# Optimization experiments

Hardware: AMD Instinct MI355X
Metric: run time of the kernel (lower is better)

## Reference

```python
import jax, jax.numpy as jnp
import numpy as np

KH, KW = 3, 3
SH, SW = 1, 1
IC, OC = 32, 32
M = 4
P = M * M
ITERS = 3
LAM = 1.0
EPS = 1e-8


def _patches(t, kh, kw, sh, sw):
    # t: [B, H, W, ...] -> [B, Ho, Wo, kh, kw, ...] (im2col, matches torch unfold+permute)
    H, W = t.shape[1], t.shape[2]
    Ho = (H - kh) // sh + 1
    Wo = (W - kw) // sw + 1
    i = (jnp.arange(Ho) * sh)[:, None] + jnp.arange(kh)[None, :]  # [Ho,kh]
    j = (jnp.arange(Wo) * sw)[:, None] + jnp.arange(kw)[None, :]  # [Wo,kw]
    tp = t[:, i]            # [B,Ho,kh,W,...]
    tp = tp[:, :, :, j]     # [B,Ho,kh,Wo,kw,...]
    return jnp.moveaxis(tp, 2, 3)  # [B,Ho,Wo,kh,kw,...]


def setup_inputs() -> dict:
    key = jax.random.key(0)
    k1, k2, k3, k4, k5 = jax.random.split(key, 5)
    x = jax.random.normal(k1, (4, 14, 14, IC, M, M), dtype=jnp.float32)
    a = jax.random.uniform(k2, (4, 14, 14, IC), dtype=jnp.float32)
    W = jax.random.uniform(k3, (KH, KW, IC, OC, M, M), dtype=jnp.float32)   # torch.rand init
    beta_u = jax.random.uniform(k4, (1, OC, 1), dtype=jnp.float32)
    beta_a = jax.random.uniform(k5, (1, OC), dtype=jnp.float32)
    return {"x": x, "a": a, "W": W, "beta_u": beta_u, "beta_a": beta_a}


def reference(x, a, W, beta_u, beta_a):
    # im2col patches
    xp = _patches(x, KH, KW, SH, SW)          # [B,Ho,Wo,kh,kw,IC,M,M]
    ap = _patches(a, KH, KW, SH, SW)          # [B,Ho,Wo,kh,kw,IC]
    # pose-transform votes: per (kh,kw,inCap,outCap) 4x4 matmul
    V = jnp.einsum('bhwklcxy,klcoyz->bhwklcoxz', xp, W)
    B, Ho, Wo = V.shape[:3]
    N = KH * KW * IC
    V = V.reshape(B, Ho, Wo, N, OC, P)        # votes
    a_in = ap.reshape(B, Ho, Wo, N)
    bu = beta_u.reshape(OC, 1)
    ba = beta_a.reshape(OC)

    # EM routing (Hinton et al. 2018, fixed inverse temperature)
    R = jnp.full((B, Ho, Wo, N, OC), 1.0 / OC, dtype=V.dtype)
    for it in range(ITERS):
        Ra = R * a_in[..., None]                                  # [B,Ho,Wo,N,OC]
        Rs = Ra.sum(axis=3) + EPS                                 # [B,Ho,Wo,OC]
        mu = jnp.einsum('bhwno,bhwnop->bhwop', Ra, V) / Rs[..., None]
        d = V - mu[:, :, :, None]                                 # [B,Ho,Wo,N,OC,P]
        sig2 = jnp.einsum('bhwno,bhwnop->bhwop', Ra, d * d) / Rs[..., None] + EPS
        cost = (bu + 0.5 * jnp.log(sig2)) * Rs[..., None]         # [B,Ho,Wo,OC,P]
        a_out = jax.nn.sigmoid(LAM * (ba - cost.sum(-1)))         # [B,Ho,Wo,OC]
        if it < ITERS - 1:
            logp = -0.5 * jnp.sum(d * d / sig2[:, :, :, None] + jnp.log(sig2)[:, :, :, None], axis=-1)
            R = jax.nn.softmax(jnp.log(a_out + EPS)[:, :, :, None] + logp, axis=-1)

    pose = mu.reshape(B, Ho, Wo, OC, M, M)
    return pose, a_out
```

## Files before the change

### kernel.cpp

```cpp
#include <hip/hip_runtime.h>


#define EPSV 1e-8f

template <int CTRL>
__device__ __forceinline__ float dppf(float v) {
  return __int_as_float(__builtin_amdgcn_update_dpp(
      0, __float_as_int(v), CTRL, 0xf, 0xf, true));
}
__device__ __forceinline__ float swz16(float v) {
  return __int_as_float(__builtin_amdgcn_ds_swizzle(__float_as_int(v), 0x401F));
}
__device__ __forceinline__ float red_max32(float v) {
  v = fmaxf(v, dppf<0xB1>(v));
  v = fmaxf(v, dppf<0x4E>(v));
  v = fmaxf(v, dppf<0x141>(v));
  v = fmaxf(v, dppf<0x140>(v));
  v = fmaxf(v, swz16(v));
  return v;
}
__device__ __forceinline__ float red_sum32(float v) {
  v += dppf<0xB1>(v);
  v += dppf<0x4E>(v);
  v += dppf<0x141>(v);
  v += dppf<0x140>(v);
  v += swz16(v);
  return v;
}

__device__ __forceinline__ void compute_votes(const float* __restrict__ Wt,
                                              const float* __restrict__ xr,
                                              int n, int o, float* __restrict__ V)
{
  float Wf[16];
  {
    const float* wp = Wt + (((n << 5) + o) << 4);
#pragma unroll
    for (int i = 0; i < 4; ++i) {
      const float4 q = *(const float4*)(wp + (i << 2));
      Wf[i*4+0]=q.x; Wf[i*4+1]=q.y; Wf[i*4+2]=q.z; Wf[i*4+3]=q.w;
    }
  }
  float xv[16];
#pragma unroll
  for (int i = 0; i < 4; ++i) {
    const float4 q = *(const float4*)(xr + (i << 2));
    xv[i*4+0]=q.x; xv[i*4+1]=q.y; xv[i*4+2]=q.z; xv[i*4+3]=q.w;
  }
#pragma unroll
  for (int xi = 0; xi < 4; ++xi)
#pragma unroll
    for (int z = 0; z < 4; ++z)
      V[xi*4+z] = fmaf(xv[xi*4+0], Wf[z],
                  fmaf(xv[xi*4+1], Wf[4+z],
                  fmaf(xv[xi*4+2], Wf[8+z],
                       xv[xi*4+3]* Wf[12+z])));
}

__global__ __launch_bounds__(512, 4) void caps_stats(
    const float* __restrict__ X, const float* __restrict__ A, const float* __restrict__ Wt,
    const float* __restrict__ Bu, const float* __restrict__ Ba,
    const float* __restrict__ prev, float* __restrict__ cur, int it)
{
  __shared__ float xp_s[144*16];
  __shared__ float a_s[144];
  __shared__ float part[8*544];
  __shared__ float prs[8*32];
  __shared__ float mu_t[512], isig_t[512], lsig_t[512];
  __shared__ float la_s[32], slog_s[32], rs_s[32];

  const int t    = threadIdx.x;
  const int o    = t & 31;
  const int ng   = t >> 5;
  const int wv   = t >> 6;
  const int lane = t & 63;

  const int bid  = blockIdx.x;
  const int pos  = bid >> 1;
  const int half = bid & 1;
  const int b  = pos / 144;
  const int r_ = pos - b*144;
  const int h  = r_ / 12;
  const int w  = r_ - (r_/12)*12;
  const int nbase = half * 144;

  for (int i = t; i < 576; i += 512) {
    const int r  = i >> 2, q4 = i & 3;
    const int n  = nbase + r;
    const int kl = n >> 5, c = n & 31;
    const int hy = h + kl/3, wx = w + (kl - (kl/3)*3);
    const float4 v = *(const float4*)(X + ((((b*14+hy)*14+wx) << 9) + (c << 4) + (q4 << 2)));
    *(float4*)(xp_s + (r << 4) + (q4 << 2)) = v;
  }
  if (t < 144) {
    const int n  = nbase + t;
    const int kl = n >> 5, c = n & 31;
    const int hy = h + kl/3, wx = w + (kl - (kl/3)*3);
    a_s[t] = A[((b*14+hy)*14+wx)*32 + c];
  }

  float mu_r[16], isig_r[16];
  float la_r = 0.f, slog_r = 0.f;

  if (it > 0) {
    {
      const int pi = t >> 5, oo = t & 31;
      const float* h0 = prev + (pos*2+0)*1056;
      const float* h1 = prev + (pos*2+1)*1056;
      const int idx = pi*32 + oo;
      const float s1   = h0[idx]       + h1[idx];
      const float s2   = h0[512+idx]   + h1[512+idx];
      const float rsum = h0[1024+oo]   + h1[1024+oo] + EPSV;
      const float mu = s1 / rsum;
      float var = s2 / rsum - mu*mu;
      var = fmaxf(var, 0.f);
      const float sg = var + EPSV;
      mu_t[idx]   = mu;
      isig_t[idx] = 1.0f / sg;
      lsig_t[idx] = __logf(sg);
      if (pi == 0) rs_s[oo] = rsum;
    }
    __syncthreads();
    if (t < 32) {
      float slog = 0.f;
#pragma unroll
      for (int p = 0; p < 16; ++p) slog += lsig_t[p*32 + t];
      const float cost = rs_s[t] * (16.0f*Bu[t] + 0.5f*slog);
      const float av = 1.0f / (1.0f + __expf(-(Ba[t] - cost)));
      la_s[t]   = __logf(av + EPSV);
      slog_s[t] = slog;
    }
    __syncthreads();
#pragma unroll
    for (int p = 0; p < 16; ++p) { mu_r[p] = mu_t[p*32 + o]; isig_r[p] = isig_t[p*32 + o]; }
    slog_r = slog_s[o];
    la_r   = la_s[o];
  } else {
#pragma unroll
    for (int p = 0; p < 16; ++p) { mu_r[p] = 0.f; isig_r[p] = 0.f; }
    __syncthreads();
  }

  float S1[16], S2[16];
#pragma unroll
  for (int p = 0; p < 16; ++p) { S1[p] = 0.f; S2[p] = 0.f; }
  float rs = 0.f;

#pragma unroll 1
  for (int j = 0; j < 9; ++j) {
    const int nl = ng + (j << 4);
    const int n  = nbase + nl;
    float V[16];
    compute_votes(Wt, xp_s + (nl << 4), n, o, V);

    float ra;
    if (it == 0) {
      ra = a_s[nl] * (1.0f/32.0f);
    } else {
      float q0 = 0.f, q1 = 0.f, q2 = 0.f, q3 = 0.f;
#pragma unroll
      for (int p = 0; p < 4; ++p) {
        float d;
        d = V[p]    - mu_r[p];    q0 = fmaf(d*d, isig_r[p],    q0);
        d = V[p+4]  - mu_r[p+4];  q1 = fmaf(d*d, isig_r[p+4],  q1);
        d = V[p+8]  - mu_r[p+8];  q2 = fmaf(d*d, isig_r[p+8],  q2);
        d = V[p+12] - mu_r[p+12]; q3 = fmaf(d*d, isig_r[p+12], q3);
      }
      const float q = slog_r + ((q0 + q1) + (q2 + q3));
      const float z = la_r - 0.5f*q;
      const float m  = red_max32(z);
      const float ev = __expf(z - m);
      const float s  = red_sum32(ev);
      ra = (ev / s) * a_s[nl];
    }
    rs += ra;
#pragma unroll
    for (int p = 0; p < 16; ++p) {
      const float rv = ra * V[p];
      S1[p] += rv;
      S2[p] = fmaf(rv, V[p], S2[p]);
    }
  }

#pragma unroll
  for (int p = 0; p < 16; ++p) {
    S1[p] += __shfl_xor(S1[p], 32);
    S2[p] += __shfl_xor(S2[p], 32);
  }
  rs += __shfl_xor(rs, 32);

  float* dst = cur + bid*1056;

  if (lane < 32) {
    float* p1 = part + wv*544 + o*17;
#pragma unroll
    for (int p = 0; p < 16; ++p) p1[p] = S1[p];
    prs[wv*32 + o] = rs;
  }
  __syncthreads();
  {
    const int pi = t >> 5, oo = t & 31;
    float s1 = 0.f;
#pragma unroll
    for (int g = 0; g < 8; ++g) s1 += part[g*544 + oo*17 + pi];
    dst[t] = s1;
    if (t < 32) {
      float r = 0.f;
#pragma unroll
      for (int g = 0; g < 8; ++g) r += prs[(g << 5) + t];
      dst[1024 + t] = r;
    }
  }
  __syncthreads();

  if (lane < 32) {
    float* p2 = part + wv*544 + o*17;
#pragma unroll
    for (int p = 0; p < 16; ++p) p2[p] = S2[p];
  }
  __syncthreads();
  {
    const int pi = t >> 5, oo = t & 31;
    float s2 = 0.f;
#pragma unroll
    for (int g = 0; g < 8; ++g) s2 += part[g*544 + oo*17 + pi];
    dst[512 + t] = s2;
  }
}

__global__ __launch_bounds__(512, 4) void caps_final(
    const float* __restrict__ prev, const float* __restrict__ Bu,
    const float* __restrict__ Ba, float* __restrict__ Out)
{
  __shared__ float mu_t[512], lsig_t[512], rs_s[32], aout_s[32];

  const int t   = threadIdx.x;
  const int pos = blockIdx.x;
  {
    const int pi = t >> 5, oo = t & 31;
    const float* h0 = prev + (pos*2+0)*1056;
    const float* h1 = prev + (pos*2+1)*1056;
    const int idx = pi*32 + oo;
    const float s1   = h0[idx]     + h1[idx];
    const float s2   = h0[512+idx] + h1[512+idx];
    const float rsum = h0[1024+oo] + h1[1024+oo] + EPSV;
    const float mu = s1 / rsum;
    float var = s2 / rsum - mu*mu;
    var = fmaxf(var, 0.f);
    mu_t[idx]   = mu;
    lsig_t[idx] = __logf(var + EPSV);
    if (pi == 0) rs_s[oo] = rsum;
  }
  __syncthreads();
  if (t < 32) {
    float slog = 0.f;
#pragma unroll
    for (int p = 0; p < 16; ++p) slog += lsig_t[p*32 + t];
    const float cost = rs_s[t] * (16.0f*Bu[t] + 0.5f*slog);
    aout_s[t] = 1.0f / (1.0f + __expf(-(Ba[t] - cost)));
  }
  __syncthreads();
  {
    const int oo = t >> 4, pi = t & 15;
    Out[pos*512 + t] = mu_t[pi*32 + oo];
  }
  if (t < 32) Out[294912 + pos*32 + t] = aout_s[t];
}

extern "C" void kernel_launch(void* const* d_in, const int* in_sizes, int n_in,
                              void* d_out, int out_size, void* d_ws, size_t ws_size,
                              hipStream_t stream) {
  (void)in_sizes; (void)n_in; (void)ws_size; (void)out_size;
  const float* X  = (const float*)d_in[0];
  const float* A  = (const float*)d_in[1];
  const float* Wt = (const float*)d_in[2];
  const float* Bu = (const float*)d_in[3];
  const float* Ba = (const float*)d_in[4];
  float* Out = (float*)d_out;

  float* pa = (float*)d_ws;
  float* pb = pa + 1152*1056;

  hipLaunchKernelGGL(caps_stats, dim3(1152), dim3(512), 0, stream,
                     X, A, Wt, Bu, Ba, (const float*)nullptr, pa, 0);
  hipLaunchKernelGGL(caps_stats, dim3(1152), dim3(512), 0, stream,
                     X, A, Wt, Bu, Ba, pa, pb, 1);
  hipLaunchKernelGGL(caps_stats, dim3(1152), dim3(512), 0, stream,
                     X, A, Wt, Bu, Ba, pb, pa, 2);
  hipLaunchKernelGGL(caps_final, dim3(576), dim3(512), 0, stream,
                     pa, Bu, Ba, Out);
}
```

Before: 162.4 us.

## Process two output positions per block and redundantly compute routing stats per thread

Each block now covers two spatial positions (one per half of the threads) for the same N-half, halving the grid. Each thread reloads the previous partial sums as float4 vectors and recomputes mu, inverse variance and activation in registers, which removes the shared-memory staging and two barriers. The partial-sum layout is transposed to o-major so these vector loads and the final output write are contiguous. The price is each thread doing 16 divides and logs redundantly, plus a loop with twice the trip count per thread and a smaller grid.

```diff
diff --git a/kernel.cpp b/kernel.cpp
--- a/kernel.cpp
+++ b/kernel.cpp
@@ -62,84 +62,83 @@
     const float* __restrict__ Bu, const float* __restrict__ Ba,
     const float* __restrict__ prev, float* __restrict__ cur, int it)
 {
-  __shared__ float xp_s[144*16];
-  __shared__ float a_s[144];
+  __shared__ float xp_s[2*144*16];
+  __shared__ float a_s[2*144];
   __shared__ float part[8*544];
   __shared__ float prs[8*32];
-  __shared__ float mu_t[512], isig_t[512], lsig_t[512];
-  __shared__ float la_s[32], slog_s[32], rs_s[32];
 
   const int t    = threadIdx.x;
   const int o    = t & 31;
-  const int ng   = t >> 5;
+  const int ng   = (t >> 5) & 7;
+  const int ph   = t >> 8;
   const int wv   = t >> 6;
   const int lane = t & 63;
 
-  const int bid  = blockIdx.x;
-  const int pos  = bid >> 1;
-  const int half = bid & 1;
-  const int b  = pos / 144;
-  const int r_ = pos - b*144;
-  const int h  = r_ / 12;
-  const int w  = r_ - (r_/12)*12;
+  const int bid   = blockIdx.x;
+  const int pair  = bid >> 1;
+  const int half  = bid & 1;
   const int nbase = half * 144;
-
-  for (int i = t; i < 576; i += 512) {
-    const int r  = i >> 2, q4 = i & 3;
-    const int n  = nbase + r;
+  const int mypos = pair*2 + ph;
+
+  for (int i = t; i < 1152; i += 512) {
+    const int pp  = (i >= 576) ? 1 : 0;
+    const int loc = i - pp*576;
+    const int r   = loc >> 2, q4 = loc & 3;
+    const int pos = pair*2 + pp;
+    const int b = pos/144, r_ = pos - b*144, h = r_/12, w = r_ - (r_/12)*12;
+    const int n = nbase + r;
     const int kl = n >> 5, c = n & 31;
     const int hy = h + kl/3, wx = w + (kl - (kl/3)*3);
     const float4 v = *(const float4*)(X + ((((b*14+hy)*14+wx) << 9) + (c << 4) + (q4 << 2)));
-    *(float4*)(xp_s + (r << 4) + (q4 << 2)) = v;
-  }
-  if (t < 144) {
-    const int n  = nbase + t;
+    *(float4*)(xp_s + pp*2304 + (r << 4) + (q4 << 2)) = v;
+  }
+  if (t < 288) {
+    const int pp  = (t >= 144) ? 1 : 0;
+    const int r   = t - pp*144;
+    const int pos = pair*2 + pp;
+    const int b = pos/144, r_ = pos - b*144, h = r_/12, w = r_ - (r_/12)*12;
+    const int n = nbase + r;
     const int kl = n >> 5, c = n & 31;
     const int hy = h + kl/3, wx = w + (kl - (kl/3)*3);
-    a_s[t] = A[((b*14+hy)*14+wx)*32 + c];
+    a_s[pp*144 + r] = A[((b*14+hy)*14+wx)*32 + c];
   }
 
   float mu_r[16], isig_r[16];
   float la_r = 0.f, slog_r = 0.f;
-
   if (it > 0) {
-    {
-      const int pi = t >> 5, oo = t & 31;
-      const float* h0 = prev + (pos*2+0)*1056;
-      const float* h1 = prev + (pos*2+1)*1056;
-      const int idx = pi*32 + oo;
-      const float s1   = h0[idx]       + h1[idx];
-      const float s2   = h0[512+idx]   + h1[512+idx];
-      const float rsum = h0[1024+oo]   + h1[1024+oo] + EPSV;
-      const float mu = s1 / rsum;
-      float var = s2 / rsum - mu*mu;
+    const float* b0 = prev + (mypos*2 + 0)*1056;
+    const float* b1 = prev + (mypos*2 + 1)*1056;
+    float s1[16], s2[16];
+#pragma unroll
+    for (int k = 0; k < 4; ++k) {
+      const float4 u0 = *(const float4*)(b0 + (o << 4) + (k << 2));
+      const float4 u1 = *(const float4*)(b1 + (o << 4) + (k << 2));
+      s1[k*4+0]=u0.x+u1.x; s1[k*4+1]=u0.y+u1.y; s1[k*4+2]=u0.z+u1.z; s1[k*4+3]=u0.w+u1.w;
+      const float4 v0 = *(const float4*)(b0 + 512 + (o << 4) + (k << 2));
+      const float4 v1 = *(const float4*)(b1 + 512 + (o << 4) + (k << 2));
+      s2[k*4+0]=v0.x+v1.x; s2[k*4+1]=v0.y+v1.y; s2[k*4+2]=v0.z+v1.z; s2[k*4+3]=v0.w+v1.w;
+    }
+    const float rsum = b0[1024+o] + b1[1024+o] + EPSV;
+    float slog = 0.f;
+#pragma unroll
+    for (int p = 0; p < 16; ++p) {
+      const float mu = s1[p] / rsum;
+      float var = s2[p] / rsum - mu*mu;
       var = fmaxf(var, 0.f);
       const float sg = var + EPSV;
-      mu_t[idx]   = mu;
-      isig_t[idx] = 1.0f / sg;
-      lsig_t[idx] = __logf(sg);
-      if (pi == 0) rs_s[oo] = rsum;
-    }
-    __syncthreads();
-    if (t < 32) {
-      float slog = 0.f;
-#pragma unroll
-      for (int p = 0; p < 16; ++p) slog += lsig_t[p*32 + t];
-      const float cost = rs_s[t] * (16.0f*Bu[t] + 0.5f*slog);
-      const float av = 1.0f / (1.0f + __expf(-(Ba[t] - cost)));
-      la_s[t]   = __logf(av + EPSV);
-      slog_s[t] = slog;
-    }
-    __syncthreads();
-#pragma unroll
-    for (int p = 0; p < 16; ++p) { mu_r[p] = mu_t[p*32 + o]; isig_r[p] = isig_t[p*32 + o]; }
-    slog_r = slog_s[o];
-    la_r   = la_s[o];
+      mu_r[p]   = mu;
+      isig_r[p] = 1.0f / sg;
+      slog     += __logf(sg);
+    }
+    const float cost = rsum * (16.0f*Bu[o] + 0.5f*slog);
+    const float av = 1.0f / (1.0f + __expf(-(Ba[o] - cost)));
+    la_r   = __logf(av + EPSV);
+    slog_r = slog;
   } else {
 #pragma unroll
     for (int p = 0; p < 16; ++p) { mu_r[p] = 0.f; isig_r[p] = 0.f; }
-    __syncthreads();
-  }
+  }
+  __syncthreads();
 
   float S1[16], S2[16];
 #pragma unroll
@@ -147,15 +146,15 @@
   float rs = 0.f;
 
 #pragma unroll 1
-  for (int j = 0; j < 9; ++j) {
-    const int nl = ng + (j << 4);
+  for (int j = 0; j < 18; ++j) {
+    const int nl = ng + (j << 3);
     const int n  = nbase + nl;
     float V[16];
-    compute_votes(Wt, xp_s + (nl << 4), n, o, V);
+    compute_votes(Wt, xp_s + ph*2304 + (nl << 4), n, o, V);
 
     float ra;
     if (it == 0) {
-      ra = a_s[nl] * (1.0f/32.0f);
+      ra = a_s[ph*144 + nl] * (1.0f/32.0f);
     } else {
       float q0 = 0.f, q1 = 0.f, q2 = 0.f, q3 = 0.f;
 #pragma unroll
@@ -171,7 +170,7 @@
       const float m  = red_max32(z);
       const float ev = __expf(z - m);
       const float s  = red_sum32(ev);
-      ra = (ev / s) * a_s[nl];
+      ra = (ev / s) * a_s[ph*144 + nl];
     }
     rs += ra;
 #pragma unroll
@@ -189,7 +188,8 @@
   }
   rs += __shfl_xor(rs, 32);
 
-  float* dst = cur + bid*1056;
+  float* seg0 = cur + ((pair*2 + 0)*2 + half)*1056;
+  float* seg1 = cur + ((pair*2 + 1)*2 + half)*1056;
 
   if (lane < 32) {
     float* p1 = part + wv*544 + o*17;
@@ -198,18 +198,20 @@
     prs[wv*32 + o] = rs;
   }
   __syncthreads();
-  {
-    const int pi = t >> 5, oo = t & 31;
-    float s1 = 0.f;
-#pragma unroll
-    for (int g = 0; g < 8; ++g) s1 += part[g*544 + oo*17 + pi];
-    dst[t] = s1;
-    if (t < 32) {
-      float r = 0.f;
-#pragma unroll
-      for (int g = 0; g < 8; ++g) r += prs[(g << 5) + t];
-      dst[1024 + t] = r;
-    }
+  for (int c = t; c < 1024; c += 512) {
+    const int pc = c >> 9, idx = c & 511;
+    const int pi = idx >> 5, oo = idx & 31;
+    float s = 0.f;
+#pragma unroll
+    for (int g = 0; g < 4; ++g) s += part[(pc*4 + g)*544 + oo*17 + pi];
+    (pc ? seg1 : seg0)[(oo << 4) + pi] = s;
+  }
+  if (t < 64) {
+    const int pc = t >> 5, oo = t & 31;
+    float r = 0.f;
+#pragma unroll
+    for (int g = 0; g < 4; ++g) r += prs[(pc*4 + g)*32 + oo];
+    (pc ? seg1 : seg0)[1024 + oo] = r;
   }
   __syncthreads();
 
@@ -219,12 +221,13 @@
     for (int p = 0; p < 16; ++p) p2[p] = S2[p];
   }
   __syncthreads();
-  {
-    const int pi = t >> 5, oo = t & 31;
-    float s2 = 0.f;
-#pragma unroll
-    for (int g = 0; g < 8; ++g) s2 += part[g*544 + oo*17 + pi];
-    dst[512 + t] = s2;
+  for (int c = t; c < 1024; c += 512) {
+    const int pc = c >> 9, idx = c & 511;
+    const int pi = idx >> 5, oo = idx & 31;
+    float s = 0.f;
+#pragma unroll
+    for (int g = 0; g < 4; ++g) s += part[(pc*4 + g)*544 + oo*17 + pi];
+    (pc ? seg1 : seg0)[512 + (oo << 4) + pi] = s;
   }
 }
 
@@ -232,38 +235,33 @@
     const float* __restrict__ prev, const float* __restrict__ Bu,
     const float* __restrict__ Ba, float* __restrict__ Out)
 {
-  __shared__ float mu_t[512], lsig_t[512], rs_s[32], aout_s[32];
+  __shared__ float lsig_t[512];
+  __shared__ float rs_s[32], aout_s[32];
 
   const int t   = threadIdx.x;
   const int pos = blockIdx.x;
-  {
-    const int pi = t >> 5, oo = t & 31;
-    const float* h0 = prev + (pos*2+0)*1056;
-    const float* h1 = prev + (pos*2+1)*1056;
-    const int idx = pi*32 + oo;
-    const float s1   = h0[idx]     + h1[idx];
-    const float s2   = h0[512+idx] + h1[512+idx];
-    const float rsum = h0[1024+oo] + h1[1024+oo] + EPSV;
-    const float mu = s1 / rsum;
-    float var = s2 / rsum - mu*mu;
-    var = fmaxf(var, 0.f);
-    mu_t[idx]   = mu;
-    lsig_t[idx] = __logf(var + EPSV);
-    if (pi == 0) rs_s[oo] = rsum;
-  }
+  const float* h0 = prev + (pos*2 + 0)*1056;
+  const float* h1 = prev + (pos*2 + 1)*1056;
+
+  const int oo = t >> 4;
+  const float rsum = h0[1024+oo] + h1[1024+oo] + EPSV;
+  const float s1 = h0[t]     + h1[t];
+  const float s2 = h0[512+t] + h1[512+t];
+  const float mu = s1 / rsum;
+  float var = s2 / rsum - mu*mu;
+  var = fmaxf(var, 0.f);
+  lsig_t[t] = __logf(var + EPSV);
+  if ((t & 15) == 0) rs_s[oo] = rsum;
   __syncthreads();
   if (t < 32) {
     float slog = 0.f;
 #pragma unroll
-    for (int p = 0; p < 16; ++p) slog += lsig_t[p*32 + t];
+    for (int p = 0; p < 16; ++p) slog += lsig_t[(t << 4) + p];
     const float cost = rs_s[t] * (16.0f*Bu[t] + 0.5f*slog);
     aout_s[t] = 1.0f / (1.0f + __expf(-(Ba[t] - cost)));
   }
   __syncthreads();
-  {
-    const int oo = t >> 4, pi = t & 15;
-    Out[pos*512 + t] = mu_t[pi*32 + oo];
-  }
+  Out[pos*512 + t] = mu;
   if (t < 32) Out[294912 + pos*32 + t] = aout_s[t];
 }
 
@@ -281,11 +279,11 @@
   float* pa = (float*)d_ws;
   float* pb = pa + 1152*1056;
 
-  hipLaunchKernelGGL(caps_stats, dim3(1152), dim3(512), 0, stream,
+  hipLaunchKernelGGL(caps_stats, dim3(576), dim3(512), 0, stream,
                      X, A, Wt, Bu, Ba, (const float*)nullptr, pa, 0);
-  hipLaunchKernelGGL(caps_stats, dim3(1152), dim3(512), 0, stream,
+  hipLaunchKernelGGL(caps_stats, dim3(576), dim3(512), 0, stream,
                      X, A, Wt, Bu, Ba, pa, pb, 1);
-  hipLaunchKernelGGL(caps_stats, dim3(1152), dim3(512), 0, stream,
+  hipLaunchKernelGGL(caps_stats, dim3(576), dim3(512), 0, stream,
                      X, A, Wt, Bu, Ba, pb, pa, 2);
   hipLaunchKernelGGL(caps_final, dim3(576), dim3(512), 0, stream,
                      pa, Bu, Ba, Out);
```

After: 191.9 us. 18.2% more time.
